# Optimization experiments

Measured on AMD Instinct MI355X. Metric: run time of the kernel, lower is better.

## Reference

```python
import jax, jax.numpy as jnp
from jax import lax
import numpy as np

P = 9          # patch_size (hardcoded in CUTSEncoder)
HALF = P // 2  # 4
EPS = 1e-5     # BatchNorm eps (torch default)
SLOPE = 0.01   # LeakyReLU negative slope (torch default)


def _conv(x, w, b):
    # 3x3 'same' conv, NCHW / OIHW
    y = lax.conv_general_dilated(x, w, (1, 1), 'SAME',
                                 dimension_numbers=('NCHW', 'OIHW', 'NCHW'))
    return y + b[None, :, None, None]


def _bn(x, gamma, beta):
    # training-mode BatchNorm2d: batch statistics over (N,H,W)
    m = jnp.mean(x, axis=(0, 2, 3), keepdims=True)
    v = jnp.var(x, axis=(0, 2, 3), keepdims=True)
    return gamma[None, :, None, None] * (x - m) * lax.rsqrt(v + EPS) + beta[None, :, None, None]


def _block(x, w, b, g, be):
    return jax.nn.leaky_relu(_bn(_conv(x, w, b), g, be), SLOPE)


def setup_inputs() -> dict:
    key = jax.random.key(0)
    ks = jax.random.split(key, 16)
    B, C, H, W = 8, 3, 256, 256
    K = 32                 # num_kernels
    L = K * 8              # latent_dim = 256
    S = 32                 # sampled_patches_per_image

    x = jax.random.normal(ks[0], (B, C, H, W), jnp.float32)
    anchors_hw = jax.random.randint(ks[1], (B, S, 2), HALF, H - HALF, jnp.int32)
    positives_hw = jax.random.randint(ks[2], (B, S, 2), HALF, H - HALF, jnp.int32)

    def w_(k, shape):
        return jax.random.normal(k, shape, jnp.float32) * 0.05

    params = {
        'w1': w_(ks[3], (K, C, 3, 3)),       'b1': jnp.zeros((K,), jnp.float32),
        'g1': jnp.ones((K,), jnp.float32),   'be1': jnp.zeros((K,), jnp.float32),
        'w2': w_(ks[4], (2 * K, K, 3, 3)),   'b2': jnp.zeros((2 * K,), jnp.float32),
        'g2': jnp.ones((2 * K,), jnp.float32), 'be2': jnp.zeros((2 * K,), jnp.float32),
        'w3': w_(ks[5], (4 * K, 2 * K, 3, 3)), 'b3': jnp.zeros((4 * K,), jnp.float32),
        'g3': jnp.ones((4 * K,), jnp.float32), 'be3': jnp.zeros((4 * K,), jnp.float32),
        'w4': w_(ks[6], (8 * K, 4 * K, 3, 3)), 'b4': jnp.zeros((8 * K,), jnp.float32),
        'g4': jnp.ones((8 * K,), jnp.float32), 'be4': jnp.zeros((8 * K,), jnp.float32),
        'rw': w_(ks[7], (S * C * P * P, S * L)),  # recon Linear [out,in]
        'rb': jnp.zeros((S * C * P * P,), jnp.float32),
    }
    return dict(x=x, anchors_hw=anchors_hw, positives_hw=positives_hw, **params)


def reference(x, anchors_hw, positives_hw,
              w1, b1, g1, be1, w2, b2, g2, be2,
              w3, b3, g3, be3, w4, b4, g4, be4, rw, rb):
    B, C, H, W = x.shape
    # 4-stage conv+BN+LeakyReLU backbone -> z: [B, L, H, W]
    z = _block(x, w1, b1, g1, be1)
    z = _block(z, w2, b2, g2, be2)
    z = _block(z, w3, b3, g3, be3)
    z = _block(z, w4, b4, g4, be4)

    # batched 9x9 patch extraction around anchors: [B, S, C, P, P]
    def patch(img, hw):  # img: [C,H,W], hw: [2]
        return lax.dynamic_slice(img, (0, hw[0] - HALF, hw[1] - HALF), (C, P, P))
    x_anchors = jax.vmap(lambda img, hws: jax.vmap(lambda hw: patch(img, hw))(hws))(x, anchors_hw)

    # batched pointwise latent gathers: [B, S, L]
    def gather_z(zb, hws):  # zb: [L,H,W]
        return zb[:, hws[:, 0], hws[:, 1]].T  # [S, L]
    z_anchors = jax.vmap(gather_z)(z, anchors_hw)
    z_positives = jax.vmap(gather_z)(z, positives_hw)

    x_anchors_flat = x_anchors.reshape(B, -1)
    x_recon = z_anchors.reshape(B, -1) @ rw.T + rb
    return (z, x_anchors_flat, x_recon, z_anchors, z_positives)
```

## Files before the change

### kernel.cpp

```cpp
#include <hip/hip_runtime.h>
#include <hip/hip_bf16.h>

#define HW 65536
constexpr int IMG_W = 256;

typedef __attribute__((ext_vector_type(8))) short short8;
typedef __attribute__((ext_vector_type(4))) float f32x4;

__device__ __forceinline__ float bf2f(unsigned short u) {
    return __uint_as_float(((unsigned)u) << 16);
}
__device__ __forceinline__ unsigned short f2bf(float f) {
    __hip_bfloat16 h = __float2bfloat16(f);
    return *reinterpret_cast<unsigned short*>(&h);
}

__global__ __launch_bounds__(256) void conv1_direct(
    const float* __restrict__ x, const float* __restrict__ wt,
    const float* __restrict__ bias, unsigned short* __restrict__ outraw)
{
    constexpr int CIN = 3, COUT = 32, OCB = 16;
    const int tile = blockIdx.x;
    const int ty0 = (tile >> 3) << 5;
    const int tx0 = (tile & 7) << 5;
    const int oc0 = blockIdx.y * OCB;
    const int b = blockIdx.z;

    __shared__ alignas(16) float s_in[CIN][34][36];
    __shared__ alignas(16) float s_w[CIN][9][OCB];

    const int tid = threadIdx.x;
    const int lx = tid & 31;
    const int ly = tid >> 5;

    float acc[4][OCB];
    #pragma unroll
    for (int j = 0; j < 4; ++j)
        #pragma unroll
        for (int oc = 0; oc < OCB; ++oc) acc[j][oc] = 0.f;

    for (int idx = tid; idx < CIN * 34 * 34; idx += 256) {
        int ic  = idx / (34 * 34);
        int rem = idx - ic * (34 * 34);
        int r   = rem / 34;
        int cc  = rem - r * 34;
        int gy = ty0 - 1 + r, gx = tx0 - 1 + cc;
        float v = 0.f;
        if ((unsigned)gy < 256u && (unsigned)gx < 256u)
            v = x[((size_t)(b * CIN + ic)) * HW + (size_t)gy * IMG_W + gx];
        s_in[ic][r][cc] = v;
    }
    for (int idx = tid; idx < CIN * 9 * OCB; idx += 256) {
        int oc  = idx & (OCB - 1);
        int t2  = idx >> 4;
        int tap = t2 % 9;
        int ic  = t2 / 9;
        s_w[ic][tap][oc] = wt[((size_t)(oc0 + oc) * CIN + ic) * 9 + tap];
    }
    __syncthreads();

    for (int ic = 0; ic < CIN; ++ic) {
        #pragma unroll
        for (int tap = 0; tap < 9; ++tap) {
            const int dy = tap / 3, dx = tap % 3;
            float wr[OCB];
            #pragma unroll
            for (int q = 0; q < OCB / 4; ++q)
                *(float4*)&wr[q * 4] = *(const float4*)&s_w[ic][tap][q * 4];
            #pragma unroll
            for (int j = 0; j < 4; ++j) {
                float iv = s_in[ic][ly + 8 * j + dy][lx + dx];
                #pragma unroll
                for (int oc = 0; oc < OCB; ++oc) acc[j][oc] += iv * wr[oc];
            }
        }
    }

    #pragma unroll
    for (int j = 0; j < 4; ++j) {
        const size_t p = ((size_t)b << 16) + (size_t)((ty0 + ly + 8 * j) << 8) + tx0 + lx;
        short8 v0, v1;
        #pragma unroll
        for (int k = 0; k < 8; ++k) {
            v0[k] = (short)f2bf(acc[j][k] + bias[oc0 + k]);
            v1[k] = (short)f2bf(acc[j][8 + k] + bias[oc0 + 8 + k]);
        }
        *(short8*)&outraw[p * COUT + oc0]     = v0;
        *(short8*)&outraw[p * COUT + oc0 + 8] = v1;
    }
}

__global__ void repack2(const float* __restrict__ w, unsigned short* __restrict__ wp,
                        int COUT, int CIN)
{
    int i = blockIdx.x * 256 + threadIdx.x;
    int K9 = 9 * CIN;
    if (i >= COUT * K9) return;
    int oc = i / K9, k = i - oc * K9;
    int tap = k / CIN, ic = k - tap * CIN;
    wp[(size_t)(k >> 3) * COUT * 8 + oc * 8 + (k & 7)] =
        f2bf(w[((size_t)(oc * CIN + ic)) * 9 + tap]);
}

template<int CIN, int COUT, int WM, int WN, int WOC>
__global__ __launch_bounds__(256, 2) void conv_mfma3(
    const unsigned short* __restrict__ in, const float2* __restrict__ coef,
    const unsigned short* __restrict__ wp, const float* __restrict__ bias,
    unsigned short* __restrict__ outraw, float2* __restrict__ partial)
{
    static_assert(WN * WOC == COUT, "block must cover full COUT");
    constexpr int CINP = CIN + 8;
    constexpr int ROWS = WM * 4;
    constexpr int NOCT = CIN / 8;
    constexpr int NG = WOC / 16;
    constexpr int ICB = CIN / 32;
    constexpr int TILES = (256 / ROWS) * 16;
    constexpr int NCHUNK = TILES * 8;

    __shared__ alignas(16) short s_in[(ROWS + 2) * 18 * CINP];
    __shared__ float2 s_coef[CIN];
    __shared__ float2 s_stat[4][128];

    const int tile = blockIdx.x;
    const int b = blockIdx.z;
    const int ty0 = (tile >> 4) * ROWS;
    const int tx0 = (tile & 15) * 16;
    const int tid = threadIdx.x;

    if (tid < CIN) s_coef[tid] = coef[tid];
    __syncthreads();

    const size_t bbase = (size_t)b << 16;
    for (int idx = tid; idx < (ROWS + 2) * 18 * NOCT; idx += 256) {
        int ic8 = idx % NOCT;
        int rc  = idx / NOCT;
        int c = rc % 18, r = rc / 18;
        int gy = ty0 - 1 + r, gx = tx0 - 1 + c;
        short8 v = (short8)0;
        if ((unsigned)gy < 256u && (unsigned)gx < 256u) {
            short8 rawv = *(const short8*)&in[(bbase + (size_t)(gy << 8) + gx) * CIN + ic8 * 8];
            #pragma unroll
            for (int j = 0; j < 8; ++j) {
                float2 ab = s_coef[ic8 * 8 + j];
                float xv = fmaf(ab.x, bf2f((unsigned short)rawv[j]), ab.y);
                xv = fmaxf(xv, 0.01f * xv);
                v[j] = (short)f2bf(xv);
            }
        }
        *(short8*)&s_in[(r * 18 + c) * CINP + ic8 * 8] = v;
    }
    __syncthreads();

    const int lane = tid & 63;
    const int wv = tid >> 6;
    const int wm = wv / WN, wn = wv % WN;
    const int ln = lane & 15;
    const int grp = lane >> 4;

    f32x4 acc[4][NG] = {};

    const unsigned short* wpb = wp + ((size_t)grp * COUT + wn * WOC + ln) * 8;

    for (int tap = 0; tap < 9; ++tap) {
        const int dy = tap / 3, dx = tap - dy * 3;
        const int arow = (wm * 4 + dy) * 18 + ln + dx;
        const int kc0 = tap * (CIN / 8);
        #pragma unroll
        for (int icb = 0; icb < ICB; ++icb) {
            short8 wfr[NG];
            #pragma unroll
            for (int g = 0; g < NG; ++g)
                wfr[g] = *(const short8*)&wpb[((size_t)(kc0 + icb * 4) * COUT + g * 16) * 8];
            #pragma unroll
            for (int f = 0; f < 4; ++f) {
                short8 px = *(const short8*)&s_in[(arow + f * 18) * CINP + icb * 32 + grp * 8];
                #pragma unroll
                for (int g = 0; g < NG; ++g)
                    acc[f][g] = __builtin_amdgcn_mfma_f32_16x16x32_bf16(wfr[g], px, acc[f][g], 0, 0, 0);
            }
        }
    }

    #pragma unroll
    for (int g = 0; g < NG; ++g) {
        const int ocl = wn * WOC + g * 16 + grp * 4;
        const f32x4 bias4 = *(const f32x4*)&bias[ocl];
        f32x4 vs = {}, vq = {};
        #pragma unroll
        for (int f = 0; f < 4; ++f) {
            const int row = ty0 + wm * 4 + f;
            f32x4 v = acc[f][g] + bias4;
            vs += v; vq += v * v;
            short4 sv;
            sv.x = (short)f2bf(v[0]); sv.y = (short)f2bf(v[1]);
            sv.z = (short)f2bf(v[2]); sv.w = (short)f2bf(v[3]);
            *(short4*)&outraw[(bbase + (size_t)(row << 8) + tx0 + ln) * COUT + ocl] = sv;
        }
        #pragma unroll
        for (int d = 1; d < 16; d <<= 1) {
            #pragma unroll
            for (int r = 0; r < 4; ++r) {
                vs[r] += __shfl_xor(vs[r], d);
                vq[r] += __shfl_xor(vq[r], d);
            }
        }
        if (ln == 0) {
            #pragma unroll
            for (int r = 0; r < 4; ++r)
                s_stat[wv][g * 16 + grp * 4 + r] = make_float2(vs[r], vq[r]);
        }
    }
    __syncthreads();
    if (tid < COUT) {
        const int wn_o = tid / WOC, ol = tid - wn_o * WOC;
        float sx = 0.f, sq = 0.f;
        #pragma unroll
        for (int m = 0; m < WM; ++m) {
            float2 p = s_stat[m * WN + wn_o][ol];
            sx += p.x; sq += p.y;
        }
        partial[(size_t)tid * NCHUNK + b * TILES + tile] = make_float2(sx, sq);
    }
}

template<int C>
__global__ __launch_bounds__(256) void bn_stats_nhwc(const unsigned short* __restrict__ raw,
                                                     float2* __restrict__ partial)
{
    constexpr int CPT = C / 8;
    constexpr int PPI = 256 / CPT;
    const int t = threadIdx.x;
    const int co = t % CPT, pg = t / CPT;
    const int p0 = blockIdx.x * 2048;
    float s[8], ss[8];
    #pragma unroll
    for (int j = 0; j < 8; ++j) { s[j] = 0.f; ss[j] = 0.f; }
    for (int p = p0 + pg; p < p0 + 2048; p += PPI) {
        short8 v = *(const short8*)&raw[(size_t)p * C + co * 8];
        #pragma unroll
        for (int j = 0; j < 8; ++j) {
            float xv = bf2f((unsigned short)v[j]);
            s[j] += xv; ss[j] += xv * xv;
        }
    }
    __shared__ float rs[256][8], rss[256][8];
    #pragma unroll
    for (int j = 0; j < 8; ++j) { rs[t][j] = s[j]; rss[t][j] = ss[j]; }
    __syncthreads();
    for (int off = PPI / 2; off > 0; off >>= 1) {
        if (pg < off) {
            #pragma unroll
            for (int j = 0; j < 8; ++j) {
                rs[t][j]  += rs[t + off * CPT][j];
                rss[t][j] += rss[t + off * CPT][j];
            }
        }
        __syncthreads();
    }
    if (pg == 0) {
        #pragma unroll
        for (int j = 0; j < 8; ++j)
            partial[(size_t)(co * 8 + j) * 256 + blockIdx.x] = make_float2(rs[t][j], rss[t][j]);
    }
}

__global__ void bn_finalize_kernel(const float2* __restrict__ partial,
                                   const float* __restrict__ gamma,
                                   const float* __restrict__ beta,
                                   float2* __restrict__ coef, int C, int nchunk)
{
    int c = threadIdx.x;
    if (c >= C) return;
    float s = 0.f, ss = 0.f;
    for (int i = 0; i < nchunk; ++i) {
        float2 p = partial[(size_t)c * nchunk + i];
        s += p.x; ss += p.y;
    }
    const float N = 524288.f;
    float m = s / N;
    float v = ss / N - m * m;
    float rsq = rsqrtf(v + 1e-5f);
    float a = gamma[c] * rsq;
    coef[c] = make_float2(a, beta[c] - m * a);
}

template<int NCHUNK>
__global__ __launch_bounds__(256) void bn_finalize2(const float2* __restrict__ partial,
                                                    const float* __restrict__ gamma,
                                                    const float* __restrict__ beta,
                                                    float2* __restrict__ coef)
{
    const int c = blockIdx.x, t = threadIdx.x;
    float s = 0.f, q = 0.f;
    for (int i = t; i < NCHUNK; i += 256) {
        float2 p = partial[(size_t)c * NCHUNK + i];
        s += p.x; q += p.y;
    }
    __shared__ float rs[256], rq[256];
    rs[t] = s; rq[t] = q;
    __syncthreads();
    for (int off = 128; off; off >>= 1) {
        if (t < off) { rs[t] += rs[t + off]; rq[t] += rq[t + off]; }
        __syncthreads();
    }
    if (t == 0) {
        const float N = 524288.f;
        float m = rs[0] / N;
        float v = rq[0] / N - m * m;
        float a = gamma[c] * rsqrtf(v + 1e-5f);
        coef[c] = make_float2(a, beta[c] - m * a);
    }
}

__global__ __launch_bounds__(256) void apply_t(const unsigned short* __restrict__ raw,
                                               const float2* __restrict__ coef,
                                               float* __restrict__ z)
{
    __shared__ float s_t[256 * 36];
    __shared__ float2 s_c[256];
    const int t = threadIdx.x;
    s_c[t] = coef[t];
    __syncthreads();

    const size_t p0 = (size_t)blockIdx.x * 32;
    const int o = t & 31, prow = t >> 5;
    #pragma unroll
    for (int it = 0; it < 4; ++it) {
        const int pxi = prow + it * 8;
        short8 v = *(const short8*)&raw[(p0 + pxi) * 256 + o * 8];
        #pragma unroll
        for (int j = 0; j < 8; ++j) {
            const int oc = o * 8 + j;
            float2 ab = s_c[oc];
            float xv = fmaf(ab.x, bf2f((unsigned short)v[j]), ab.y);
            xv = fmaxf(xv, 0.01f * xv);
            s_t[oc * 36 + (pxi ^ ((o & 7) * 4))] = xv;
        }
    }
    __syncthreads();

    const int Q = t & 7, ocr = t >> 3;
    const int b = (int)(p0 >> 16);
    const int pxl = (int)(p0 & 65535);
    #pragma unroll
    for (int pass = 0; pass < 8; ++pass) {
        const int oc = ocr + pass * 32;
        const int w = (oc >> 3) & 7;
        f32x4 vv = *(const f32x4*)&s_t[oc * 36 + ((Q ^ w) * 4)];
        *(f32x4*)&z[(((size_t)(b * 256 + oc)) << 16) + pxl + Q * 4] = vv;
    }
}

__global__ void patches_kernel(const float* __restrict__ x, const int* __restrict__ hw,
                               float* __restrict__ out)
{
    int bs = blockIdx.x;
    int b = bs >> 5;
    int h = hw[bs * 2], w = hw[bs * 2 + 1];
    int t = threadIdx.x;
    if (t < 243) {
        int c = t / 81, r = (t / 9) % 9, cc = t % 9;
        out[(size_t)bs * 243 + t] =
            x[((size_t)(b * 3 + c)) * HW + (size_t)(h - 4 + r) * IMG_W + (w - 4 + cc)];
    }
}

__global__ void gather_kernel(const float* __restrict__ z, const int* __restrict__ hw,
                              float* __restrict__ out)
{
    int bs = blockIdx.x;
    int b = bs >> 5;
    int h = hw[bs * 2], w = hw[bs * 2 + 1];
    int l = threadIdx.x;
    out[(size_t)bs * 256 + l] = z[((size_t)(b * 256 + l)) * HW + (size_t)h * IMG_W + w];
}

__global__ __launch_bounds__(256) void recon_kernel(const float* __restrict__ za,
                                                    const float* __restrict__ rw,
                                                    const float* __restrict__ rb,
                                                    float* __restrict__ out)
{
    int wave = threadIdx.x >> 6, lane = threadIdx.x & 63;
    int n0 = blockIdx.x * 16 + wave * 4;
    float acc[4][8];
    #pragma unroll
    for (int j = 0; j < 4; ++j)
        #pragma unroll
        for (int bb = 0; bb < 8; ++bb) acc[j][bb] = 0.f;

    for (int i = 0; i < 32; ++i) {
        int k = i * 256 + lane * 4;
        float4 wv[4];
        #pragma unroll
        for (int j = 0; j < 4; ++j)
            wv[j] = *(const float4*)&rw[(size_t)(n0 + j) * 8192 + k];
        #pragma unroll
        for (int bb = 0; bb < 8; ++bb) {
            float4 zv = *(const float4*)&za[(size_t)bb * 8192 + k];
            #pragma unroll
            for (int j = 0; j < 4; ++j)
                acc[j][bb] += zv.x * wv[j].x + zv.y * wv[j].y + zv.z * wv[j].z + zv.w * wv[j].w;
        }
    }
    #pragma unroll
    for (int j = 0; j < 4; ++j)
        #pragma unroll
        for (int bb = 0; bb < 8; ++bb) {
            float v = acc[j][bb];
            #pragma unroll
            for (int off = 32; off; off >>= 1) v += __shfl_down(v, off);
            if (lane == 0) out[(size_t)bb * 7776 + n0 + j] = v + rb[n0 + j];
        }
}

extern "C" void kernel_launch(void* const* d_in, const int* in_sizes, int n_in,
                              void* d_out, int out_size, void* d_ws, size_t ws_size,
                              hipStream_t stream) {
    (void)in_sizes; (void)n_in; (void)out_size; (void)ws_size;

    const float* x        = (const float*)d_in[0];
    const int* anchors    = (const int*)d_in[1];
    const int* positives  = (const int*)d_in[2];
    const float* w1 = (const float*)d_in[3];  const float* b1 = (const float*)d_in[4];
    const float* g1 = (const float*)d_in[5];  const float* be1 = (const float*)d_in[6];
    const float* w2 = (const float*)d_in[7];  const float* b2 = (const float*)d_in[8];
    const float* g2 = (const float*)d_in[9];  const float* be2 = (const float*)d_in[10];
    const float* w3 = (const float*)d_in[11]; const float* b3 = (const float*)d_in[12];
    const float* g3 = (const float*)d_in[13]; const float* be3 = (const float*)d_in[14];
    const float* w4 = (const float*)d_in[15]; const float* b4 = (const float*)d_in[16];
    const float* g4 = (const float*)d_in[17]; const float* be4 = (const float*)d_in[18];
    const float* rw = (const float*)d_in[19]; const float* rb = (const float*)d_in[20];

    float* z  = (float*)d_out;
    float* xa = z + 134217728;
    float* xr = xa + 62208;
    float* za = xr + 62208;
    float* zp = za + 65536;

    char* zb = (char*)d_out;
    unsigned short* raw1 = (unsigned short*)zb;
    unsigned short* raw2 = (unsigned short*)(zb + 33554432ull);
    unsigned short* raw3 = (unsigned short*)(zb + 100663296ull);

    char* ws = (char*)d_ws;
    unsigned short* wp   = (unsigned short*)ws;
    float2* partial = (float2*)(ws + 1048576ull);
    float2* coef1   = (float2*)(ws + 10485760ull);
    float2* coef2   = coef1 + 256;
    float2* coef3   = coef2 + 256;
    float2* coef4   = coef3 + 256;
    unsigned short* raw4 = (unsigned short*)(ws + 16777216ull);

    conv1_direct<<<dim3(64, 2, 8), 256, 0, stream>>>(x, w1, b1, raw1);
    bn_stats_nhwc<32><<<256, 256, 0, stream>>>(raw1, partial);
    bn_finalize_kernel<<<1, 256, 0, stream>>>(partial, g1, be1, coef1, 32, 256);

    repack2<<<(64 * 288 + 255) / 256, 256, 0, stream>>>(w2, wp, 64, 32);
    conv_mfma3<32, 64, 4, 1, 64><<<dim3(256, 1, 8), 256, 0, stream>>>(raw1, coef1, wp, b2, raw2, partial);
    bn_finalize2<2048><<<64, 256, 0, stream>>>(partial, g2, be2, coef2);

    repack2<<<(128 * 576 + 255) / 256, 256, 0, stream>>>(w3, wp, 128, 64);
    conv_mfma3<64, 128, 4, 1, 128><<<dim3(256, 1, 8), 256, 0, stream>>>(raw2, coef2, wp, b3, raw3, partial);
    bn_finalize2<2048><<<128, 256, 0, stream>>>(partial, g3, be3, coef3);

    repack2<<<(256 * 1152 + 255) / 256, 256, 0, stream>>>(w4, wp, 256, 128);
    conv_mfma3<128, 256, 2, 2, 128><<<dim3(512, 1, 8), 256, 0, stream>>>(raw3, coef3, wp, b4, raw4, partial);
    bn_finalize2<4096><<<256, 256, 0, stream>>>(partial, g4, be4, coef4);

    apply_t<<<16384, 256, 0, stream>>>(raw4, coef4, z);

    patches_kernel<<<256, 256, 0, stream>>>(x, anchors, xa);
    gather_kernel<<<256, 256, 0, stream>>>(z, anchors, za);
    gather_kernel<<<256, 256, 0, stream>>>(z, positives, zp);
    recon_kernel<<<486, 256, 0, stream>>>(za, rw, rb, xr);
}
```

Baseline: 828.9 us.

## Switch conv MFMA to 32x32x16 tiles and stage output through swizzled LDS

The implicit-GEMM conv kernels now use 32x32x16 bf16 MFMA instructions instead of 16x16x32, with each wave covering two 32-pixel blocks that share each weight fragment. This halves how often weight fragments are reloaded per pixel. The epilogue writes bf16 results into a reused, XOR-swizzled LDS buffer and then stores them to global memory as coalesced 16-byte chunks, replacing the scattered 8-byte stores. Per-layer occupancy hints are added (3 waves minimum for layer 2), at the cost of more accumulator registers per wave and an extra LDS round trip.

```diff
diff --git a/kernel.cpp b/kernel.cpp
--- a/kernel.cpp
+++ b/kernel.cpp
@@ -6,6 +6,7 @@
 
 typedef __attribute__((ext_vector_type(8))) short short8;
 typedef __attribute__((ext_vector_type(4))) float f32x4;
+typedef __attribute__((ext_vector_type(16))) float f32x16;
 
 __device__ __forceinline__ float bf2f(unsigned short u) {
     return __uint_as_float(((unsigned)u) << 16);
@@ -102,22 +103,25 @@
         f2bf(w[((size_t)(oc * CIN + ic)) * 9 + tap]);
 }
 
-template<int CIN, int COUT, int WM, int WN, int WOC>
-__global__ __launch_bounds__(256, 2) void conv_mfma3(
+template<int CIN, int COUT, int WM, int WN, int WOC, int MINW>
+__global__ __launch_bounds__(256, MINW) void conv_mfma4(
     const unsigned short* __restrict__ in, const float2* __restrict__ coef,
     const unsigned short* __restrict__ wp, const float* __restrict__ bias,
     unsigned short* __restrict__ outraw, float2* __restrict__ partial)
 {
-    static_assert(WN * WOC == COUT, "block must cover full COUT");
+    static_assert(WM * WN == 4 && WN * WOC == COUT, "bad wave geometry");
     constexpr int CINP = CIN + 8;
     constexpr int ROWS = WM * 4;
     constexpr int NOCT = CIN / 8;
-    constexpr int NG = WOC / 16;
-    constexpr int ICB = CIN / 32;
-    constexpr int TILES = (256 / ROWS) * 16;
+    constexpr int NG = WOC / 32;
+    constexpr int KS = CIN / 16;
+    constexpr int TILES = 65536 / (ROWS * 16);
     constexpr int NCHUNK = TILES * 8;
-
-    __shared__ alignas(16) short s_in[(ROWS + 2) * 18 * CINP];
+    constexpr int SIN = (ROWS + 2) * 18 * CINP;
+    constexpr int SOUT = ROWS * 16 * COUT;
+    constexpr int SBUF = SIN > SOUT ? SIN : SOUT;
+
+    __shared__ alignas(16) short s_buf[SBUF];
     __shared__ float2 s_coef[CIN];
     __shared__ float2 s_stat[4][128];
 
@@ -147,70 +151,95 @@
                 v[j] = (short)f2bf(xv);
             }
         }
-        *(short8*)&s_in[(r * 18 + c) * CINP + ic8 * 8] = v;
+        *(short8*)&s_buf[(r * 18 + c) * CINP + ic8 * 8] = v;
     }
     __syncthreads();
 
     const int lane = tid & 63;
     const int wv = tid >> 6;
     const int wm = wv / WN, wn = wv % WN;
-    const int ln = lane & 15;
-    const int grp = lane >> 4;
-
-    f32x4 acc[4][NG] = {};
-
-    const unsigned short* wpb = wp + ((size_t)grp * COUT + wn * WOC + ln) * 8;
-
+    const int n5 = lane & 31;
+    const int kg = lane >> 5;
+
+    f32x16 acc[2][NG] = {};
+
+    const int r0 = wm * 4 + (n5 >> 4);
+    const int c0 = n5 & 15;
+    const unsigned short* wpb = wp + ((size_t)kg * COUT + wn * WOC + n5) * 8;
+
+    #pragma unroll
     for (int tap = 0; tap < 9; ++tap) {
         const int dy = tap / 3, dx = tap - dy * 3;
-        const int arow = (wm * 4 + dy) * 18 + ln + dx;
-        const int kc0 = tap * (CIN / 8);
-        #pragma unroll
-        for (int icb = 0; icb < ICB; ++icb) {
-            short8 wfr[NG];
-            #pragma unroll
-            for (int g = 0; g < NG; ++g)
-                wfr[g] = *(const short8*)&wpb[((size_t)(kc0 + icb * 4) * COUT + g * 16) * 8];
-            #pragma unroll
-            for (int f = 0; f < 4; ++f) {
-                short8 px = *(const short8*)&s_in[(arow + f * 18) * CINP + icb * 32 + grp * 8];
+        const int abase = (r0 + dy) * 18 + c0 + dx;
+        #pragma unroll
+        for (int ks = 0; ks < KS; ++ks) {
+            const int koff = ks * 16 + kg * 8;
+            short8 p0 = *(const short8*)&s_buf[ abase       * CINP + koff];
+            short8 p1 = *(const short8*)&s_buf[(abase + 36) * CINP + koff];
+            const size_t wo = (size_t)(tap * (CIN / 8) + ks * 2) * COUT * 8;
+            #pragma unroll
+            for (int g = 0; g < NG; ++g) {
+                short8 wf = *(const short8*)&wpb[wo + (size_t)g * 32 * 8];
+                acc[0][g] = __builtin_amdgcn_mfma_f32_32x32x16_bf16(wf, p0, acc[0][g], 0, 0, 0);
+                acc[1][g] = __builtin_amdgcn_mfma_f32_32x32x16_bf16(wf, p1, acc[1][g], 0, 0, 0);
+            }
+        }
+    }
+
+    __syncthreads();
+    #pragma unroll
+    for (int g = 0; g < NG; ++g) {
+        #pragma unroll
+        for (int q = 0; q < 4; ++q) {
+            const int ocq = wn * WOC + g * 32 + q * 8 + kg * 4;
+            const f32x4 b4 = *(const f32x4*)&bias[ocq];
+            f32x4 v0, v1;
+            #pragma unroll
+            for (int r = 0; r < 4; ++r) { v0[r] = acc[0][g][q * 4 + r]; v1[r] = acc[1][g][q * 4 + r]; }
+            v0 += b4; v1 += b4;
+
+            const int px0 = r0 * 16 + c0;
+            const int px1 = (r0 + 2) * 16 + c0;
+            short4 s0, s1;
+            s0.x = (short)f2bf(v0[0]); s0.y = (short)f2bf(v0[1]);
+            s0.z = (short)f2bf(v0[2]); s0.w = (short)f2bf(v0[3]);
+            s1.x = (short)f2bf(v1[0]); s1.y = (short)f2bf(v1[1]);
+            s1.z = (short)f2bf(v1[2]); s1.w = (short)f2bf(v1[3]);
+            unsigned a0 = (unsigned)((px0 * COUT + ocq) * 2) ^ ((px0 & 7) << 4);
+            unsigned a1 = (unsigned)((px1 * COUT + ocq) * 2) ^ ((px1 & 7) << 4);
+            *(short4*)((char*)s_buf + a0) = s0;
+            *(short4*)((char*)s_buf + a1) = s1;
+
+            f32x4 vs = v0 + v1, vq = v0 * v0 + v1 * v1;
+            #pragma unroll
+            for (int d = 1; d < 32; d <<= 1) {
                 #pragma unroll
-                for (int g = 0; g < NG; ++g)
-                    acc[f][g] = __builtin_amdgcn_mfma_f32_16x16x32_bf16(wfr[g], px, acc[f][g], 0, 0, 0);
+                for (int r = 0; r < 4; ++r) {
+                    vs[r] += __shfl_xor(vs[r], d);
+                    vq[r] += __shfl_xor(vq[r], d);
+                }
             }
-        }
-    }
-
-    #pragma unroll
-    for (int g = 0; g < NG; ++g) {
-        const int ocl = wn * WOC + g * 16 + grp * 4;
-        const f32x4 bias4 = *(const f32x4*)&bias[ocl];
-        f32x4 vs = {}, vq = {};
-        #pragma unroll
-        for (int f = 0; f < 4; ++f) {
-            const int row = ty0 + wm * 4 + f;
-            f32x4 v = acc[f][g] + bias4;
-            vs += v; vq += v * v;
-            short4 sv;
-            sv.x = (short)f2bf(v[0]); sv.y = (short)f2bf(v[1]);
-            sv.z = (short)f2bf(v[2]); sv.w = (short)f2bf(v[3]);
-            *(short4*)&outraw[(bbase + (size_t)(row << 8) + tx0 + ln) * COUT + ocl] = sv;
-        }
-        #pragma unroll
-        for (int d = 1; d < 16; d <<= 1) {
-            #pragma unroll
-            for (int r = 0; r < 4; ++r) {
-                vs[r] += __shfl_xor(vs[r], d);
-                vq[r] += __shfl_xor(vq[r], d);
+            if (n5 == 0) {
+                #pragma unroll
+                for (int r = 0; r < 4; ++r)
+                    s_stat[wv][g * 32 + q * 8 + kg * 4 + r] = make_float2(vs[r], vq[r]);
             }
         }
-        if (ln == 0) {
-            #pragma unroll
-            for (int r = 0; r < 4; ++r)
-                s_stat[wv][g * 16 + grp * 4 + r] = make_float2(vs[r], vq[r]);
-        }
-    }
-    __syncthreads();
+    }
+    __syncthreads();
+
+    constexpr int CPP = COUT / 8;
+    constexpr int TOTCH = ROWS * 16 * CPP;
+    #pragma unroll
+    for (int i = 0; i < TOTCH / 256; ++i) {
+        const int c = tid + i * 256;
+        const int px = c / CPP, o8 = c % CPP;
+        const int row = px >> 4, col = px & 15;
+        const unsigned a = (unsigned)((px * COUT + o8 * 8) * 2) ^ ((px & 7) << 4);
+        short8 v = *(const short8*)((const char*)s_buf + a);
+        *(short8*)&outraw[(bbase + (size_t)((ty0 + row) << 8) + tx0 + col) * COUT + o8 * 8] = v;
+    }
+
     if (tid < COUT) {
         const int wn_o = tid / WOC, ol = tid - wn_o * WOC;
         float sx = 0.f, sq = 0.f;
@@ -456,15 +485,15 @@
     bn_finalize_kernel<<<1, 256, 0, stream>>>(partial, g1, be1, coef1, 32, 256);
 
     repack2<<<(64 * 288 + 255) / 256, 256, 0, stream>>>(w2, wp, 64, 32);
-    conv_mfma3<32, 64, 4, 1, 64><<<dim3(256, 1, 8), 256, 0, stream>>>(raw1, coef1, wp, b2, raw2, partial);
+    conv_mfma4<32, 64, 4, 1, 64, 3><<<dim3(256, 1, 8), 256, 0, stream>>>(raw1, coef1, wp, b2, raw2, partial);
     bn_finalize2<2048><<<64, 256, 0, stream>>>(partial, g2, be2, coef2);
 
     repack2<<<(128 * 576 + 255) / 256, 256, 0, stream>>>(w3, wp, 128, 64);
-    conv_mfma3<64, 128, 4, 1, 128><<<dim3(256, 1, 8), 256, 0, stream>>>(raw2, coef2, wp, b3, raw3, partial);
+    conv_mfma4<64, 128, 4, 1, 128, 2><<<dim3(256, 1, 8), 256, 0, stream>>>(raw2, coef2, wp, b3, raw3, partial);
     bn_finalize2<2048><<<128, 256, 0, stream>>>(partial, g3, be3, coef3);
 
     repack2<<<(256 * 1152 + 255) / 256, 256, 0, stream>>>(w4, wp, 256, 128);
-    conv_mfma3<128, 256, 2, 2, 128><<<dim3(512, 1, 8), 256, 0, stream>>>(raw3, coef3, wp, b4, raw4, partial);
+    conv_mfma4<128, 256, 2, 2, 128, 2><<<dim3(512, 1, 8), 256, 0, stream>>>(raw3, coef3, wp, b4, raw4, partial);
     bn_finalize2<4096><<<256, 256, 0, stream>>>(partial, g4, be4, coef4);
 
     apply_t<<<16384, 256, 0, stream>>>(raw4, coef4, z);
```

Result: slower. 1.071 ms (+29.2%).

## Prefetch conv input into registers, write per-wave BN partials, retune conv geometry

Applied to the files above, without the earlier changes.

The conv kernel now issues all global loads of its input halo into registers before the first barrier, so the fetch overlaps the wait for the BN coefficients. The BN-apply step then runs from registers into LDS. BN partial sums are written per wave straight to global memory in a chunk-major layout, which removes the shared-memory reduction and its extra barrier. The finalize kernel reads that transposed layout, and the workspace offsets are moved to fit the larger partial buffer. Layer 3 switches to a 2x2 wave geometry with more blocks, and occupancy hints are raised to 3 for layers 2 and 3, which risks register pressure and forces finalize to reduce four times as many partials.

```diff
diff --git a/kernel.cpp b/kernel.cpp
--- a/kernel.cpp
+++ b/kernel.cpp
@@ -102,24 +102,24 @@
         f2bf(w[((size_t)(oc * CIN + ic)) * 9 + tap]);
 }
 
-template<int CIN, int COUT, int WM, int WN, int WOC>
-__global__ __launch_bounds__(256, 2) void conv_mfma3(
+template<int CIN, int COUT, int WM, int WN, int WOC, int MINW>
+__global__ __launch_bounds__(256, MINW) void conv_mfma5(
     const unsigned short* __restrict__ in, const float2* __restrict__ coef,
     const unsigned short* __restrict__ wp, const float* __restrict__ bias,
     unsigned short* __restrict__ outraw, float2* __restrict__ partial)
 {
-    static_assert(WN * WOC == COUT, "block must cover full COUT");
+    static_assert(WM * WN == 4 && WN * WOC == COUT, "bad wave geometry");
     constexpr int CINP = CIN + 8;
     constexpr int ROWS = WM * 4;
     constexpr int NOCT = CIN / 8;
     constexpr int NG = WOC / 16;
     constexpr int ICB = CIN / 32;
-    constexpr int TILES = (256 / ROWS) * 16;
-    constexpr int NCHUNK = TILES * 8;
+    constexpr int TILES = 65536 / (ROWS * 16);
+    constexpr int NCH = (ROWS + 2) * 18 * NOCT;
+    constexpr int CPT = (NCH + 255) / 256;
 
     __shared__ alignas(16) short s_in[(ROWS + 2) * 18 * CINP];
     __shared__ float2 s_coef[CIN];
-    __shared__ float2 s_stat[4][128];
 
     const int tile = blockIdx.x;
     const int b = blockIdx.z;
@@ -128,26 +128,42 @@
     const int tid = threadIdx.x;
 
     if (tid < CIN) s_coef[tid] = coef[tid];
-    __syncthreads();
 
     const size_t bbase = (size_t)b << 16;
-    for (int idx = tid; idx < (ROWS + 2) * 18 * NOCT; idx += 256) {
-        int ic8 = idx % NOCT;
-        int rc  = idx / NOCT;
-        int c = rc % 18, r = rc / 18;
-        int gy = ty0 - 1 + r, gx = tx0 - 1 + c;
-        short8 v = (short8)0;
-        if ((unsigned)gy < 256u && (unsigned)gx < 256u) {
-            short8 rawv = *(const short8*)&in[(bbase + (size_t)(gy << 8) + gx) * CIN + ic8 * 8];
-            #pragma unroll
-            for (int j = 0; j < 8; ++j) {
-                float2 ab = s_coef[ic8 * 8 + j];
-                float xv = fmaf(ab.x, bf2f((unsigned short)rawv[j]), ab.y);
-                xv = fmaxf(xv, 0.01f * xv);
-                v[j] = (short)f2bf(xv);
+    short8 stg[CPT];
+    #pragma unroll
+    for (int i = 0; i < CPT; ++i) {
+        const int idx = tid + i * 256;
+        const int ic8 = idx & (NOCT - 1);
+        const int rc  = idx / NOCT;
+        const int c = rc % 18, r = rc / 18;
+        const int gy = ty0 - 1 + r, gx = tx0 - 1 + c;
+        stg[i] = (short8)0;
+        if (idx < NCH && (unsigned)gy < 256u && (unsigned)gx < 256u)
+            stg[i] = *(const short8*)&in[(bbase + (size_t)(gy << 8) + gx) * CIN + ic8 * 8];
+    }
+    __syncthreads();
+
+    #pragma unroll
+    for (int i = 0; i < CPT; ++i) {
+        const int idx = tid + i * 256;
+        if (idx < NCH) {
+            const int ic8 = idx & (NOCT - 1);
+            const int rc  = idx / NOCT;
+            const int c = rc % 18, r = rc / 18;
+            const int gy = ty0 - 1 + r, gx = tx0 - 1 + c;
+            short8 v = (short8)0;
+            if ((unsigned)gy < 256u && (unsigned)gx < 256u) {
+                #pragma unroll
+                for (int j = 0; j < 8; ++j) {
+                    float2 ab = s_coef[ic8 * 8 + j];
+                    float xv = fmaf(ab.x, bf2f((unsigned short)stg[i][j]), ab.y);
+                    xv = fmaxf(xv, 0.01f * xv);
+                    v[j] = (short)f2bf(xv);
+                }
             }
-        }
-        *(short8*)&s_in[(r * 18 + c) * CINP + ic8 * 8] = v;
+            *(short8*)&s_in[(r * 18 + c) * CINP + ic8 * 8] = v;
+        }
     }
     __syncthreads();
 
@@ -181,15 +197,16 @@
         }
     }
 
+    const size_t pchunk = ((size_t)(b * TILES + tile) * WM + wm) * COUT;
     #pragma unroll
     for (int g = 0; g < NG; ++g) {
         const int ocl = wn * WOC + g * 16 + grp * 4;
-        const f32x4 bias4 = *(const f32x4*)&bias[ocl];
+        const f32x4 b4 = *(const f32x4*)&bias[ocl];
         f32x4 vs = {}, vq = {};
         #pragma unroll
         for (int f = 0; f < 4; ++f) {
             const int row = ty0 + wm * 4 + f;
-            f32x4 v = acc[f][g] + bias4;
+            f32x4 v = acc[f][g] + b4;
             vs += v; vq += v * v;
             short4 sv;
             sv.x = (short)f2bf(v[0]); sv.y = (short)f2bf(v[1]);
@@ -207,19 +224,8 @@
         if (ln == 0) {
             #pragma unroll
             for (int r = 0; r < 4; ++r)
-                s_stat[wv][g * 16 + grp * 4 + r] = make_float2(vs[r], vq[r]);
-        }
-    }
-    __syncthreads();
-    if (tid < COUT) {
-        const int wn_o = tid / WOC, ol = tid - wn_o * WOC;
-        float sx = 0.f, sq = 0.f;
-        #pragma unroll
-        for (int m = 0; m < WM; ++m) {
-            float2 p = s_stat[m * WN + wn_o][ol];
-            sx += p.x; sq += p.y;
-        }
-        partial[(size_t)tid * NCHUNK + b * TILES + tile] = make_float2(sx, sq);
+                partial[pchunk + ocl + r] = make_float2(vs[r], vq[r]);
+        }
     }
 }
 
@@ -284,8 +290,8 @@
     coef[c] = make_float2(a, beta[c] - m * a);
 }
 
-template<int NCHUNK>
-__global__ __launch_bounds__(256) void bn_finalize2(const float2* __restrict__ partial,
+template<int C, int NCHUNK>
+__global__ __launch_bounds__(256) void bn_finalize3(const float2* __restrict__ partial,
                                                     const float* __restrict__ gamma,
                                                     const float* __restrict__ beta,
                                                     float2* __restrict__ coef)
@@ -293,7 +299,7 @@
     const int c = blockIdx.x, t = threadIdx.x;
     float s = 0.f, q = 0.f;
     for (int i = t; i < NCHUNK; i += 256) {
-        float2 p = partial[(size_t)c * NCHUNK + i];
+        float2 p = partial[(size_t)i * C + c];
         s += p.x; q += p.y;
     }
     __shared__ float rs[256], rq[256];
@@ -445,27 +451,27 @@
     char* ws = (char*)d_ws;
     unsigned short* wp   = (unsigned short*)ws;
     float2* partial = (float2*)(ws + 1048576ull);
-    float2* coef1   = (float2*)(ws + 10485760ull);
+    float2* coef1   = (float2*)(ws + 17825792ull);
     float2* coef2   = coef1 + 256;
     float2* coef3   = coef2 + 256;
     float2* coef4   = coef3 + 256;
-    unsigned short* raw4 = (unsigned short*)(ws + 16777216ull);
+    unsigned short* raw4 = (unsigned short*)(ws + 18874368ull);
 
     conv1_direct<<<dim3(64, 2, 8), 256, 0, stream>>>(x, w1, b1, raw1);
     bn_stats_nhwc<32><<<256, 256, 0, stream>>>(raw1, partial);
     bn_finalize_kernel<<<1, 256, 0, stream>>>(partial, g1, be1, coef1, 32, 256);
 
     repack2<<<(64 * 288 + 255) / 256, 256, 0, stream>>>(w2, wp, 64, 32);
-    conv_mfma3<32, 64, 4, 1, 64><<<dim3(256, 1, 8), 256, 0, stream>>>(raw1, coef1, wp, b2, raw2, partial);
-    bn_finalize2<2048><<<64, 256, 0, stream>>>(partial, g2, be2, coef2);
+    conv_mfma5<32, 64, 4, 1, 64, 3><<<dim3(256, 1, 8), 256, 0, stream>>>(raw1, coef1, wp, b2, raw2, partial);
+    bn_finalize3<64, 8192><<<64, 256, 0, stream>>>(partial, g2, be2, coef2);
 
     repack2<<<(128 * 576 + 255) / 256, 256, 0, stream>>>(w3, wp, 128, 64);
-    conv_mfma3<64, 128, 4, 1, 128><<<dim3(256, 1, 8), 256, 0, stream>>>(raw2, coef2, wp, b3, raw3, partial);
-    bn_finalize2<2048><<<128, 256, 0, stream>>>(partial, g3, be3, coef3);
+    conv_mfma5<64, 128, 2, 2, 64, 3><<<dim3(512, 1, 8), 256, 0, stream>>>(raw2, coef2, wp, b3, raw3, partial);
+    bn_finalize3<128, 8192><<<128, 256, 0, stream>>>(partial, g3, be3, coef3);
 
     repack2<<<(256 * 1152 + 255) / 256, 256, 0, stream>>>(w4, wp, 256, 128);
-    conv_mfma3<128, 256, 2, 2, 128><<<dim3(512, 1, 8), 256, 0, stream>>>(raw3, coef3, wp, b4, raw4, partial);
-    bn_finalize2<4096><<<256, 256, 0, stream>>>(partial, g4, be4, coef4);
+    conv_mfma5<128, 256, 2, 2, 128, 2><<<dim3(512, 1, 8), 256, 0, stream>>>(raw3, coef3, wp, b4, raw4, partial);
+    bn_finalize3<256, 8192><<<256, 256, 0, stream>>>(partial, g4, be4, coef4);
 
     apply_t<<<16384, 256, 0, stream>>>(raw4, coef4, z);
 
```

Result: slower. 866.0 us (+4.5%).
